# Performance work log

Measured on AMD Instinct MI355X. Metric: run time of the kernel, lower is better.

## Reference

```python
import jax, jax.numpy as jnp
import numpy as np

D_MODEL = 1024
D_INNER = 2048      # expand=2
D_STATE = 128
NHEADS = 32
HEADDIM = 64
DCONV = 4
CONV_DIM = D_INNER + 2 * D_STATE                 # x, B, C channels through conv
D_IN_PROJ = 2 * D_INNER + 2 * D_STATE + NHEADS   # z, xBC, dt
NBLOCKS = 4


def _mlp(x, w1, b1, w2, b2):
    # MLP(2, in, out): Linear(in,in) -> ReLU -> Linear(in,out)
    return jax.nn.relu(x @ w1 + b1) @ w2 + b2


def _mamba2_block(u, Wi, cw, cb, dtb, Alog, Dsk, nw, Wo):
    B, L, _ = u.shape
    zxbcdt = u @ Wi                                        # [B,L,D_IN_PROJ]
    z, xBC, dt = jnp.split(zxbcdt, [D_INNER, D_INNER + CONV_DIM], axis=-1)
    # causal depthwise conv1d, kernel 4
    pad = jnp.pad(xBC, ((0, 0), (DCONV - 1, 0), (0, 0)))
    conv = cb
    for k in range(DCONV):
        conv = conv + pad[:, k:k + L, :] * cw[:, k]
    xBC = jax.nn.silu(conv)
    xh, Bm, Cm = jnp.split(xBC, [D_INNER, D_INNER + D_STATE], axis=-1)
    dt = jax.nn.softplus(dt + dtb)                         # [B,L,H]
    A = -jnp.exp(Alog)                                     # [H], negative
    xh = xh.reshape(B, L, NHEADS, HEADDIM)

    def step(h, inp):
        x_t, dt_t, b_t, c_t = inp                          # [B,H,P],[B,H],[B,N],[B,N]
        dA = jnp.exp(dt_t * A)                             # [B,H]
        h = h * dA[..., None, None] + (dt_t[..., None] * x_t)[..., None] * b_t[:, None, None, :]
        y = jnp.einsum('bhpn,bn->bhp', h, c_t)
        return h, y

    h0 = jnp.zeros((B, NHEADS, HEADDIM, D_STATE), u.dtype)
    _, ys = jax.lax.scan(step, h0, (xh.transpose(1, 0, 2, 3), dt.transpose(1, 0, 2),
                                    Bm.transpose(1, 0, 2), Cm.transpose(1, 0, 2)))
    y = ys.transpose(1, 0, 2, 3) + Dsk[None, None, :, None] * xh   # D skip per head
    y = y.reshape(B, L, D_INNER)
    y = y * jax.nn.silu(z)                                 # gated RMSNorm (gate before norm)
    y = y * jax.lax.rsqrt(jnp.mean(y * y, axis=-1, keepdims=True) + 1e-5) * nw
    return y @ Wo


def setup_inputs() -> dict:
    key = jax.random.key(0)
    ks = jax.random.split(key, 16)
    B, S, STATE = 4, 512, 510
    s = 0.02
    return {
        'x': jax.random.normal(ks[0], (B, S, STATE), jnp.float32),
        'steps_left': jax.random.uniform(ks[1], (B, S, 1), jnp.float32) * 100.0,
        'current_r': jax.random.normal(ks[2], (B, S, 1), jnp.float32),
        'mlp_in_w1': jax.random.normal(ks[3], (STATE + 2, STATE + 2), jnp.float32) * s,
        'mlp_in_b1': jnp.zeros((STATE + 2,), jnp.float32),
        'mlp_in_w2': jax.random.normal(ks[4], (STATE + 2, D_MODEL), jnp.float32) * s,
        'mlp_in_b2': jnp.zeros((D_MODEL,), jnp.float32),
        'W_in': jax.random.normal(ks[5], (NBLOCKS, D_MODEL, D_IN_PROJ), jnp.float32) * s,
        'conv_w': jax.random.normal(ks[6], (NBLOCKS, CONV_DIM, DCONV), jnp.float32) * 0.2,
        'conv_b': jnp.zeros((NBLOCKS, CONV_DIM), jnp.float32),
        'dt_bias': jax.random.normal(ks[7], (NBLOCKS, NHEADS), jnp.float32) * 0.1,
        'A_log': jnp.log(jax.random.uniform(ks[8], (NBLOCKS, NHEADS), jnp.float32, 1.0, 16.0)),
        'D_skip': jnp.ones((NBLOCKS, NHEADS), jnp.float32),
        'norm_w': jnp.ones((NBLOCKS, D_INNER), jnp.float32),
        'W_out': jax.random.normal(ks[9], (NBLOCKS, D_INNER, D_MODEL), jnp.float32) * s,
        'mlp_out_w1': jax.random.normal(ks[10], (D_MODEL, D_MODEL), jnp.float32) * s,
        'mlp_out_b1': jnp.zeros((D_MODEL,), jnp.float32),
        'mlp_out_w2': jax.random.normal(ks[11], (D_MODEL, 1), jnp.float32) * s,
        'mlp_out_b2': jnp.zeros((1,), jnp.float32),
    }


def reference(x, steps_left, current_r,
              mlp_in_w1, mlp_in_b1, mlp_in_w2, mlp_in_b2,
              W_in, conv_w, conv_b, dt_bias, A_log, D_skip, norm_w, W_out,
              mlp_out_w1, mlp_out_b1, mlp_out_w2, mlp_out_b2):
    h = jnp.concatenate([x, steps_left, current_r], axis=-1)   # [B,S,state+2]
    h = _mlp(h, mlp_in_w1, mlp_in_b1, mlp_in_w2, mlp_in_b2)
    for i in range(NBLOCKS):
        h = _mamba2_block(h, W_in[i], conv_w[i], conv_b[i], dt_bias[i],
                          A_log[i], D_skip[i], norm_w[i], W_out[i])
    return _mlp(h, mlp_out_w1, mlp_out_b1, mlp_out_w2, mlp_out_b2)  # [B,S,1]
```

## Files before the change

### kernel.cpp

```cpp
#include <hip/hip_runtime.h>
#include <hip/hip_bf16.h>
#include <math.h>

#define D_MODEL   1024
#define D_INNER   2048
#define D_STATE   128
#define NHEADS    32
#define HEADDIM   64
#define DCONV     4
#define CONV_DIM  (D_INNER + 2 * D_STATE)
#define D_IN_PROJ (2 * D_INNER + 2 * D_STATE + NHEADS)
#define NBLOCKS   4
#define BATCH     4
#define SEQ       512
#define NTOK      (BATCH * SEQ)
#define STATE_IN  510
#define NPAD_IN   4480
#define NSEG      8
#define SEGLEN    64
#define NBH       (BATCH * NHEADS)
#define OFF_B     D_INNER
#define OFF_C     (D_INNER + D_STATE)
#define OFF_DT    (D_IN_PROJ - NHEADS)

typedef _Float16 half8_t __attribute__((ext_vector_type(8)));
typedef float f32x4_t  __attribute__((ext_vector_type(4)));
typedef unsigned short us;
typedef unsigned short us8 __attribute__((ext_vector_type(8)));

__device__ __forceinline__ us f2h(float f) {
    _Float16 h = (_Float16)f;
    return __builtin_bit_cast(us, h);
}
__device__ __forceinline__ float h2f(us u) {
    return (float)__builtin_bit_cast(_Float16, u);
}
__device__ __forceinline__ void gl2lds16(const us* gp, us* lp) {
    __builtin_amdgcn_global_load_lds(
        (const __attribute__((address_space(1))) unsigned int*)(gp),
        (__attribute__((address_space(3))) unsigned int*)(lp), 16, 0, 0);
}

__global__ void concat_kernel(const float* __restrict__ x,
                              const float* __restrict__ steps,
                              const float* __restrict__ curr,
                              us* __restrict__ hcat)
{
    int idx = blockIdx.x * 256 + threadIdx.x;
    if (idx >= NTOK * 512) return;
    int bl = idx >> 9;
    int c  = idx & 511;
    float v;
    if (c < STATE_IN)       v = x[(size_t)bl * STATE_IN + c];
    else if (c == STATE_IN) v = steps[bl];
    else                    v = curr[bl];
    hcat[idx] = f2h(v);
}

#define NT_TRANS 3488
__global__ __launch_bounds__(256)
void transpose_all_kernel(const float* __restrict__ mi_w1, const float* __restrict__ mi_w2,
                          const float* __restrict__ W_in, const float* __restrict__ W_out,
                          const float* __restrict__ mo_w1,
                          us* __restrict__ wt_mi1, us* __restrict__ wt_mi2,
                          us* __restrict__ wt_in, us* __restrict__ wt_out,
                          us* __restrict__ wt_mo1)
{
    int bid = blockIdx.x;
    const float* W; us* WT; int K, N, ntx, r;
    if (bid < 32)        { W = mi_w1; WT = wt_mi1; K = 512;  N = 512;  ntx = 4; r = bid; }
    else if (bid < 96)   { W = mi_w2; WT = wt_mi2; K = 512;  N = 1024; ntx = 8; r = bid - 32; }
    else if (bid < 2336) {
        int rel = bid - 96, i = rel / 560;
        r = rel - i * 560;
        W  = W_in  + (size_t)i * D_MODEL * D_IN_PROJ;
        WT = wt_in + (size_t)i * NPAD_IN * 1024;
        K = 1024; N = D_IN_PROJ; ntx = 35;
    }
    else if (bid < 3360) {
        int rel = bid - 2336, i = rel / 256;
        r = rel - i * 256;
        W  = W_out  + (size_t)i * D_INNER * D_MODEL;
        WT = wt_out + (size_t)i * 1024 * 2048;
        K = 2048; N = 1024; ntx = 8;
    }
    else { W = mo_w1; WT = wt_mo1; K = 1024; N = 1024; ntx = 8; r = bid - 3360; }
    int n0 = (r % ntx) * 128, k0 = (r / ntx) * 64;

    int t = threadIdx.x;
    int ko = t & 7;
    int nq = t >> 3;
    int n  = n0 + nq * 4;
    int k  = k0 + ko * 8;

    float4 v[8];
    if (n < N) {
        const float* src = W + (size_t)k * N + n;
#pragma unroll
        for (int j = 0; j < 8; ++j)
            v[j] = *(const float4*)(src + (size_t)j * N);
    } else {
#pragma unroll
        for (int j = 0; j < 8; ++j) v[j] = make_float4(0.f, 0.f, 0.f, 0.f);
    }
#pragma unroll
    for (int q = 0; q < 4; ++q) {
        us8 o;
#pragma unroll
        for (int j = 0; j < 8; ++j) o[j] = f2h(((const float*)&v[j])[q]);
        *(us8*)(WT + (size_t)(n + q) * K + k) = o;
    }
}

#define PHASE(TT, CUR, STG)                                                     \
    {                                                                           \
        if ((TT) == NT - 1)                                                     \
            asm volatile("s_waitcnt vmcnt(0)" ::: "memory");                    \
        else if constexpr (BM / 64 + BN / 64 == 4)                              \
            asm volatile("s_waitcnt vmcnt(4)" ::: "memory");                    \
        else if constexpr (BM / 64 + BN / 64 == 3)                              \
            asm volatile("s_waitcnt vmcnt(3)" ::: "memory");                    \
        else                                                                    \
            asm volatile("s_waitcnt vmcnt(2)" ::: "memory");                    \
        __builtin_amdgcn_s_barrier();                                           \
        if ((TT) + 2 < NT) stage(STG, ((TT) + 2) << 5);                         \
        half8_t af[TI], bfr[4];                                                 \
        _Pragma("unroll")                                                       \
        for (int ti = 0; ti < TI; ++ti) {                                       \
            int rr = wr + ti * 16 + l16;                                        \
            af[ti] = *(const half8_t*)&Al[CUR][rr * 32 + ((g ^ ((rr >> 2) & 3)) * 8)]; \
        }                                                                       \
        _Pragma("unroll")                                                       \
        for (int tj = 0; tj < 4; ++tj) {                                        \
            int rr = wc + tj * 16 + l16;                                        \
            bfr[tj] = *(const half8_t*)&Bl[CUR][rr * 32 + ((g ^ ((rr >> 2) & 3)) * 8)]; \
        }                                                                       \
        _Pragma("unroll")                                                       \
        for (int ti = 0; ti < TI; ++ti)                                         \
            _Pragma("unroll")                                                   \
            for (int tj = 0; tj < 4; ++tj)                                      \
                acc[ti][tj] = __builtin_amdgcn_mfma_f32_16x16x32_f16(           \
                    af[ti], bfr[tj], acc[ti][tj], 0, 0, 0);                     \
    }

template<int BM, int BN, int TI>
__global__ __launch_bounds__(256)
void mfma_gemm_f16(const us* __restrict__ A, const us* __restrict__ BT,
                   const float* __restrict__ bias, us* __restrict__ C,
                   int N, int K, int relu)
{
    __shared__ __attribute__((aligned(16))) us Al[3][BM * 32];
    __shared__ __attribute__((aligned(16))) us Bl[3][BN * 32];
    const int tid = threadIdx.x, lane = tid & 63, wave = tid >> 6;
    const int g = lane >> 4, l16 = lane & 15;
    const int wr = (BN == 128) ? (wave >> 1) * 64 : wave * (BM / 4);
    const int wc = (BN == 128) ? (wave & 1) * 64 : 0;
    const int m0 = blockIdx.y * BM, n0 = blockIdx.x * BN;
    const int lrow = lane >> 2;
    const int lcol = ((lane & 3) ^ ((lrow >> 2) & 3)) * 8;

    f32x4_t acc[TI][4];
    const f32x4_t zero = {0.f, 0.f, 0.f, 0.f};
#pragma unroll
    for (int i = 0; i < TI; ++i)
#pragma unroll
        for (int j = 0; j < 4; ++j) acc[i][j] = zero;

    const us* abase = A  + (size_t)m0 * K;
    const us* bbase = BT + (size_t)n0 * K;

    auto stage = [&](int buf, int k0) {
#pragma unroll
        for (int s = 0; s < BM / 64; ++s) {
            int rb = wave * (BM / 4) + s * 16;
            gl2lds16(abase + (size_t)(rb + lrow) * K + k0 + lcol, &Al[buf][rb * 32]);
        }
#pragma unroll
        for (int s = 0; s < BN / 64; ++s) {
            int rb = wave * (BN / 4) + s * 16;
            gl2lds16(bbase + (size_t)(rb + lrow) * K + k0 + lcol, &Bl[buf][rb * 32]);
        }
    };

    const int NT = K >> 5;
    stage(0, 0);
    stage(1, 32);

    for (int t = 0; t < NT; t += 3) {
        PHASE(t, 0, 2)
        if (t + 1 < NT) PHASE(t + 1, 1, 0)
        if (t + 2 < NT) PHASE(t + 2, 2, 1)
    }

#pragma unroll
    for (int tj = 0; tj < 4; ++tj) {
        int col = n0 + wc + tj * 16 + l16;
        if (col >= N) continue;
        float bv = bias ? bias[col] : 0.f;
#pragma unroll
        for (int ti = 0; ti < TI; ++ti) {
            int rbase = m0 + wr + ti * 16 + g * 4;
#pragma unroll
            for (int r = 0; r < 4; ++r) {
                float v = acc[ti][tj][r] + bv;
                if (relu) v = fmaxf(v, 0.f);
                C[(size_t)(rbase + r) * N + col] = f2h(v);
            }
        }
    }
}

__global__ __launch_bounds__(256)
void conv_silu_kernel(const us* __restrict__ zxbcdt,
                      const float* __restrict__ cw,
                      const float* __restrict__ cb,
                      us* __restrict__ xBCc)
{
    int idx = blockIdx.x * 256 + threadIdx.x;
    if (idx >= NTOK * (CONV_DIM / 4)) return;
    int cq = idx % (CONV_DIM / 4);
    int bl = idx / (CONV_DIM / 4);
    int b  = bl >> 9;
    int l  = bl & 511;
    int c  = cq * 4;
    float4 w0 = *(const float4*)&cw[(c + 0) * DCONV];
    float4 w1 = *(const float4*)&cw[(c + 1) * DCONV];
    float4 w2 = *(const float4*)&cw[(c + 2) * DCONV];
    float4 w3 = *(const float4*)&cw[(c + 3) * DCONV];
    float4 bb = *(const float4*)&cb[c];
    float a0 = bb.x, a1 = bb.y, a2 = bb.z, a3 = bb.w;
    const us* base = zxbcdt + (size_t)(b * SEQ) * D_IN_PROJ + D_INNER + c;
#pragma unroll
    for (int k = 0; k < DCONV; ++k) {
        int ll = l + k - (DCONV - 1);
        if (ll >= 0) {
            ushort4 u = *(const ushort4*)(base + (size_t)ll * D_IN_PROJ);
            a0 = fmaf(h2f(u.x), ((const float*)&w0)[k], a0);
            a1 = fmaf(h2f(u.y), ((const float*)&w1)[k], a1);
            a2 = fmaf(h2f(u.z), ((const float*)&w2)[k], a2);
            a3 = fmaf(h2f(u.w), ((const float*)&w3)[k], a3);
        }
    }
    ushort4 o;
    o.x = f2h(a0 / (1.f + __expf(-a0)));
    o.y = f2h(a1 / (1.f + __expf(-a1)));
    o.z = f2h(a2 / (1.f + __expf(-a2)));
    o.w = f2h(a3 / (1.f + __expf(-a3)));
    *(ushort4*)(xBCc + (size_t)bl * CONV_DIM + c) = o;
}

__global__ __launch_bounds__(256)
void scan_seg_mfma_kernel(const us* __restrict__ zx, const us* __restrict__ xc,
                          const float* __restrict__ dt_bias,
                          const float* __restrict__ A_log,
                          const float* __restrict__ D_skip,
                          float* __restrict__ y, float* __restrict__ alpha,
                          us* __restrict__ Hseg)
{
    __shared__ __attribute__((aligned(16))) us Csh[64 * 128];
    __shared__ __attribute__((aligned(16))) us Bsh[64 * 128];
    __shared__ __attribute__((aligned(16))) us Bt[128 * 64];
    __shared__ __attribute__((aligned(16))) us Xt[64 * 64];
    __shared__ float dt_s[64], ls[64], csc[64];
    us* Ssh = Csh;
    const int bi = blockIdx.x, bh = bi >> 3, seg = bi & 7;
    const int b = bh >> 5, h = bh & 31;
    const int tid = threadIdx.x, lane = tid & 63, w = tid >> 6;
    const int g = lane >> 4, l16 = lane & 15;
    const int t0g = seg * SEGLEN;
    const size_t rowbase = (size_t)(b * SEQ + t0g);

    {
        int rr = lane >> 4, s = lane & 15;
#pragma unroll
        for (int it = 0; it < 4; ++it) {
            int rb = w * 16 + it * 4;
            int row = rb + rr;
            const us* src = xc + (rowbase + row) * CONV_DIM;
            int sw = (s ^ (row & 7)) * 8;
            gl2lds16(src + OFF_C + sw, &Csh[rb * 128]);
            gl2lds16(src + OFF_B + sw, &Bsh[rb * 128]);
        }
    }
#pragma unroll
    for (int qi = 0; qi < 4; ++qi) {
        int idx = tid + qi * 256;
        int pq = idx & 15, j = idx >> 4;
        ushort4 v = *(const ushort4*)(xc + (rowbase + j) * CONV_DIM + h * 64 + pq * 4);
#pragma unroll
        for (int e = 0; e < 4; ++e) {
            int p = pq * 4 + e;
            int pc = ((((j >> 3) ^ (p & 7)) << 3) | (j & 7));
            Xt[p * 64 + pc] = ((const us*)&v)[e];
        }
    }
#pragma unroll
    for (int qi = 0; qi < 8; ++qi) {
        int idx = tid + qi * 256;
        int nq = idx & 31, j = idx >> 5;
        ushort4 v = *(const ushort4*)(xc + (rowbase + j) * CONV_DIM + OFF_B + nq * 4);
#pragma unroll
        for (int e = 0; e < 4; ++e) {
            int n = nq * 4 + e;
            int pc = ((((j >> 3) ^ (n & 7)) << 3) | (j & 7));
            Bt[n * 64 + pc] = ((const us*)&v)[e];
        }
    }
    if (tid < 64) {
        int j = tid;
        float dtraw = h2f(zx[(rowbase + j) * D_IN_PROJ + OFF_DT + h]) + dt_bias[h];
        float dtv = (dtraw > 20.f) ? dtraw : log1pf(expf(dtraw));
        float ld = dtv * (-expf(A_log[h]));
#pragma unroll
        for (int o = 1; o < 64; o <<= 1) {
            float v = __shfl_up(ld, o);
            if (j >= o) ld += v;
        }
        float al = expf(ld);
        dt_s[j] = dtv;
        ls[j] = ld;
        alpha[(size_t)bh * SEQ + t0g + j] = al;
        float cend = __shfl(ld, 63);
        csc[j] = dtv * expf(cend - ld);
    }
    __syncthreads();

    const float Dsk = D_skip[h];
    const f32x4_t vzero = {0.f, 0.f, 0.f, 0.f};

    f32x4_t acc1[4];
#pragma unroll
    for (int jt = 0; jt < 4; ++jt) acc1[jt] = vzero;
    {
        int ia = w * 16 + l16;
#pragma unroll
        for (int ks = 0; ks < 4; ++ks) {
            half8_t a = *(const half8_t*)&Csh[ia * 128 + (((ks * 4 + g) ^ (ia & 7)) << 3)];
#pragma unroll
            for (int jt = 0; jt < 4; ++jt) {
                int jr = jt * 16 + l16;
                half8_t bfr = *(const half8_t*)&Bsh[jr * 128 + (((ks * 4 + g) ^ (jr & 7)) << 3)];
                acc1[jt] = __builtin_amdgcn_mfma_f32_16x16x32_f16(a, bfr, acc1[jt], 0, 0, 0);
            }
        }
    }
    __syncthreads();

    {
        int i0 = w * 16 + g * 4;
        float lsi[4];
#pragma unroll
        for (int r = 0; r < 4; ++r) lsi[r] = ls[i0 + r];
#pragma unroll
        for (int jt = 0; jt < 4; ++jt) {
            int j = jt * 16 + l16;
            float lj = ls[j], dj = dt_s[j];
#pragma unroll
            for (int r = 0; r < 4; ++r) {
                int i = i0 + r;
                float v = 0.f;
                if (j < i)       v = acc1[jt][r] * dj * __expf(lsi[r] - lj);
                else if (j == i) v = acc1[jt][r] * dj + Dsk;
                int pc = ((((j >> 3) ^ (i & 7)) << 3) | (j & 7));
                Ssh[i * 64 + pc] = f2h(v);
            }
        }
    }
    __syncthreads();

    f32x4_t acc2[4];
#pragma unroll
    for (int nt = 0; nt < 4; ++nt) acc2[nt] = vzero;
    {
        int ia = w * 16 + l16;
#pragma unroll
        for (int ks = 0; ks < 2; ++ks) {
            half8_t a = *(const half8_t*)&Ssh[ia * 64 + (((ks * 4 + g) ^ (ia & 7)) << 3)];
#pragma unroll
            for (int nt = 0; nt < 4; ++nt) {
                int pr = nt * 16 + l16;
                half8_t bfr = *(const half8_t*)&Xt[pr * 64 + (((ks * 4 + g) ^ (pr & 7)) << 3)];
                acc2[nt] = __builtin_amdgcn_mfma_f32_16x16x32_f16(a, bfr, acc2[nt], 0, 0, 0);
            }
        }
    }
    {
        int i0 = w * 16 + g * 4;
#pragma unroll
        for (int nt = 0; nt < 4; ++nt) {
            int p = nt * 16 + l16;
#pragma unroll
            for (int r = 0; r < 4; ++r)
                y[(rowbase + i0 + r) * D_INNER + h * 64 + p] = acc2[nt][r];
        }
    }
    f32x4_t acc3[8];
#pragma unroll
    for (int nt = 0; nt < 8; ++nt) acc3[nt] = vzero;
    {
        int pa = w * 16 + l16;
#pragma unroll
        for (int ks = 0; ks < 2; ++ks) {
            half8_t araw = *(const half8_t*)&Xt[pa * 64 + (((ks * 4 + g) ^ (pa & 7)) << 3)];
            half8_t a;
#pragma unroll
            for (int e = 0; e < 8; ++e)
                a[e] = (_Float16)((float)araw[e] * csc[ks * 32 + g * 8 + e]);
#pragma unroll
            for (int nt = 0; nt < 8; ++nt) {
                int nr = nt * 16 + l16;
                half8_t bfr = *(const half8_t*)&Bt[nr * 64 + (((ks * 4 + g) ^ (nr & 7)) << 3)];
                acc3[nt] = __builtin_amdgcn_mfma_f32_16x16x32_f16(a, bfr, acc3[nt], 0, 0, 0);
            }
        }
    }
    {
        int p0 = w * 16 + g * 4;
#pragma unroll
        for (int nt = 0; nt < 8; ++nt) {
            int n = nt * 16 + l16;
#pragma unroll
            for (int r = 0; r < 4; ++r)
                Hseg[((size_t)bi * 64 + p0 + r) * 128 + n] = f2h(acc3[nt][r]);
        }
    }
}

__global__ __launch_bounds__(512)
void state_fixup_kernel(const float* __restrict__ alpha, us* __restrict__ Hseg)
{
    const int bh = blockIdx.x >> 1, hf = blockIdx.x & 1;
    const int t = threadIdx.x, p = t >> 3, ng = t & 7;
    const int off = hf * 64 + ng * 8;
    float carry[8];
#pragma unroll
    for (int j = 0; j < 8; ++j) carry[j] = 0.f;
    for (int seg = 0; seg < NSEG; ++seg) {
        us* hs = Hseg + (((size_t)bh * NSEG + seg) * 64 + p) * 128 + off;
        float ae = alpha[(size_t)bh * SEQ + seg * SEGLEN + SEGLEN - 1];
        float tmp[8];
#pragma unroll
        for (int q = 0; q < 2; ++q) {
            ushort4 u = *(const ushort4*)(hs + q * 4);
            tmp[q*4+0] = h2f(u.x); tmp[q*4+1] = h2f(u.y);
            tmp[q*4+2] = h2f(u.z); tmp[q*4+3] = h2f(u.w);
        }
#pragma unroll
        for (int q = 0; q < 2; ++q) {
            ushort4 o;
            o.x = f2h(carry[q*4+0]); o.y = f2h(carry[q*4+1]);
            o.z = f2h(carry[q*4+2]); o.w = f2h(carry[q*4+3]);
            *(ushort4*)(hs + q * 4) = o;
        }
#pragma unroll
        for (int j = 0; j < 8; ++j) carry[j] = fmaf(carry[j], ae, tmp[j]);
    }
}

__global__ __launch_bounds__(256)
void correct_mfma_kernel(const us* __restrict__ xc, const float* __restrict__ alpha,
                         const us* __restrict__ Hseg, float* __restrict__ y)
{
    __shared__ __attribute__((aligned(16))) us Csh[64 * 128];
    __shared__ __attribute__((aligned(16))) us Hsh[64 * 128];
    __shared__ float als_s[64];
    const int bi = blockIdx.x;
    const int bh = bi / 7, seg = 1 + (bi % 7);
    const int b = bh >> 5, h = bh & 31;
    const int tid = threadIdx.x, lane = tid & 63, w = tid >> 6;
    const int g = lane >> 4, l16 = lane & 15;
    const int t0g = seg * SEGLEN;
    const size_t rowbase = (size_t)(b * SEQ + t0g);
    const size_t hbase = (size_t)(bh * NSEG + seg) * 64;

    {
        int rr = lane >> 4, s = lane & 15;
#pragma unroll
        for (int it = 0; it < 4; ++it) {
            int rb = w * 16 + it * 4;
            int row = rb + rr;
            int sw = (s ^ (row & 7)) * 8;
            gl2lds16(xc + (rowbase + row) * CONV_DIM + OFF_C + sw, &Csh[rb * 128]);
            gl2lds16(Hseg + (hbase + row) * 128 + sw, &Hsh[rb * 128]);
        }
    }
    if (tid < 64) als_s[tid] = alpha[(size_t)bh * SEQ + t0g + tid];
    __syncthreads();

    const f32x4_t vzero = {0.f, 0.f, 0.f, 0.f};
    f32x4_t acc[4];
#pragma unroll
    for (int nt = 0; nt < 4; ++nt) acc[nt] = vzero;
    int ia = w * 16 + l16;
#pragma unroll
    for (int ks = 0; ks < 4; ++ks) {
        half8_t a = *(const half8_t*)&Csh[ia * 128 + (((ks * 4 + g) ^ (ia & 7)) << 3)];
#pragma unroll
        for (int nt = 0; nt < 4; ++nt) {
            int pr = nt * 16 + l16;
            half8_t bfr = *(const half8_t*)&Hsh[pr * 128 + (((ks * 4 + g) ^ (pr & 7)) << 3)];
            acc[nt] = __builtin_amdgcn_mfma_f32_16x16x32_f16(a, bfr, acc[nt], 0, 0, 0);
        }
    }
    int i0 = w * 16 + g * 4;
#pragma unroll
    for (int nt = 0; nt < 4; ++nt) {
        int p = nt * 16 + l16;
#pragma unroll
        for (int r = 0; r < 4; ++r) {
            size_t idx = (rowbase + i0 + r) * D_INNER + h * 64 + p;
            y[idx] += als_s[i0 + r] * acc[nt][r];
        }
    }
}

__global__ __launch_bounds__(256)
void gated_rmsnorm_kernel(const float* __restrict__ y,
                          const us* __restrict__ zxbcdt,
                          const float* __restrict__ norm_w,
                          us* __restrict__ yn)
{
    int bl = blockIdx.x;
    int t  = threadIdx.x;
    const float* yr = y + (size_t)bl * D_INNER;
    const us* zr = zxbcdt + (size_t)bl * D_IN_PROJ;
    us* outr = yn + (size_t)bl * D_INNER;

    float gv[8];
    float ss = 0.f;
#pragma unroll
    for (int q = 0; q < 8; ++q) {
        int j = t + q * 256;
        float z = h2f(zr[j]);
        float g = yr[j] * (z / (1.f + __expf(-z)));
        gv[q] = g;
        ss += g * g;
    }
    __shared__ float red[256];
    red[t] = ss;
    __syncthreads();
    for (int w = 128; w > 0; w >>= 1) {
        if (t < w) red[t] += red[t + w];
        __syncthreads();
    }
    float rs = rsqrtf(red[0] / (float)D_INNER + 1e-5f);
#pragma unroll
    for (int q = 0; q < 8; ++q) {
        int j = t + q * 256;
        outr[j] = f2h(gv[q] * rs * norm_w[j]);
    }
}

__global__ __launch_bounds__(256)
void final_dot_kernel(const us* __restrict__ t1,
                      const float* __restrict__ w2,
                      const float* __restrict__ b2,
                      float* __restrict__ out)
{
    int bl = blockIdx.x;
    int t  = threadIdx.x;
    float s = 0.f;
    for (int j = t; j < D_MODEL; j += 256)
        s = fmaf(h2f(t1[(size_t)bl * D_MODEL + j]), w2[j], s);
    __shared__ float red[256];
    red[t] = s;
    __syncthreads();
    for (int w = 128; w > 0; w >>= 1) {
        if (t < w) red[t] += red[t + w];
        __syncthreads();
    }
    if (t == 0) out[bl] = red[0] + b2[0];
}

extern "C" void kernel_launch(void* const* d_in, const int* in_sizes, int n_in,
                              void* d_out, int out_size, void* d_ws, size_t ws_size,
                              hipStream_t stream)
{
    const float* x        = (const float*)d_in[0];
    const float* steps    = (const float*)d_in[1];
    const float* curr     = (const float*)d_in[2];
    const float* mi_w1    = (const float*)d_in[3];
    const float* mi_b1    = (const float*)d_in[4];
    const float* mi_w2    = (const float*)d_in[5];
    const float* mi_b2    = (const float*)d_in[6];
    const float* W_in     = (const float*)d_in[7];
    const float* conv_w   = (const float*)d_in[8];
    const float* conv_b   = (const float*)d_in[9];
    const float* dt_bias  = (const float*)d_in[10];
    const float* A_log    = (const float*)d_in[11];
    const float* D_skip   = (const float*)d_in[12];
    const float* norm_w   = (const float*)d_in[13];
    const float* W_out    = (const float*)d_in[14];
    const float* mo_w1    = (const float*)d_in[15];
    const float* mo_b1    = (const float*)d_in[16];
    const float* mo_w2    = (const float*)d_in[17];
    const float* mo_b2    = (const float*)d_in[18];
    float* out = (float*)d_out;

    us* wt_mi1 = (us*)d_ws;
    us* wt_mi2 = wt_mi1 + (size_t)512 * 512;
    us* wt_in  = wt_mi2 + (size_t)1024 * 512;
    us* wt_out = wt_in  + (size_t)4 * NPAD_IN * 1024;
    us* wt_mo1 = wt_out + (size_t)4 * 1024 * 2048;
    us* Hseg   = wt_mo1 + (size_t)1024 * 1024;
    us* hcat   = Hseg   + (size_t)NBH * NSEG * 64 * 128;
    us* h      = hcat   + (size_t)NTOK * 512;
    us* zxb    = h      + (size_t)NTOK * D_MODEL;
    us* xc     = zxb    + (size_t)NTOK * D_IN_PROJ;
    us* yn     = xc     + (size_t)NTOK * CONV_DIM;
    us* t0     = zxb;
    us* t1     = xc;
    float* fbase = (float*)((((uintptr_t)(yn + (size_t)NTOK * D_INNER)) + 255)
                            & ~(uintptr_t)255);
    float* y     = fbase;
    float* alpha = y + (size_t)NTOK * D_INNER;

    transpose_all_kernel<<<NT_TRANS, 256, 0, stream>>>(
        mi_w1, mi_w2, W_in, W_out, mo_w1,
        wt_mi1, wt_mi2, wt_in, wt_out, wt_mo1);

    concat_kernel<<<(NTOK * 512 + 255) / 256, 256, 0, stream>>>(x, steps, curr, hcat);

    mfma_gemm_f16<64, 64, 1><<<dim3(512/64, NTOK/64), 256, 0, stream>>>(
        hcat, wt_mi1, mi_b1, t0, 512, 512, 1);
    mfma_gemm_f16<64, 64, 1><<<dim3(1024/64, NTOK/64), 256, 0, stream>>>(
        t0, wt_mi2, mi_b2, h, 1024, 512, 0);

    for (int i = 0; i < NBLOCKS; ++i) {
        mfma_gemm_f16<128, 128, 4><<<dim3(NPAD_IN/128, NTOK/128), 256, 0, stream>>>(
            h, wt_in + (size_t)i * NPAD_IN * 1024, nullptr, zxb, D_IN_PROJ, D_MODEL, 0);
        conv_silu_kernel<<<(NTOK * (CONV_DIM/4) + 255) / 256, 256, 0, stream>>>(
            zxb, conv_w + (size_t)i * CONV_DIM * DCONV, conv_b + (size_t)i * CONV_DIM, xc);
        scan_seg_mfma_kernel<<<NBH * NSEG, 256, 0, stream>>>(
            zxb, xc, dt_bias + i * NHEADS, A_log + i * NHEADS, D_skip + i * NHEADS,
            y, alpha, Hseg);
        state_fixup_kernel<<<NBH * 2, 512, 0, stream>>>(alpha, Hseg);
        correct_mfma_kernel<<<NBH * (NSEG - 1), 256, 0, stream>>>(xc, alpha, Hseg, y);
        gated_rmsnorm_kernel<<<NTOK, 256, 0, stream>>>(
            y, zxb, norm_w + (size_t)i * D_INNER, yn);
        mfma_gemm_f16<64, 64, 1><<<dim3(1024/64, NTOK/64), 256, 0, stream>>>(
            yn, wt_out + (size_t)i * 1024 * 2048, nullptr, h, 1024, 2048, 0);
    }

    mfma_gemm_f16<64, 64, 1><<<dim3(1024/64, NTOK/64), 256, 0, stream>>>(
        h, wt_mo1, mo_b1, t1, 1024, 1024, 1);
    final_dot_kernel<<<NTOK, 256, 0, stream>>>(t1, mo_w2, mo_b2, out);
}
```

Before: 722.8 us.

## Fuse fp32 weight conversion into GEMM B-tile loads, drop transpose pre-pass

Removes the separate transpose/convert kernel that wrote fp16 transposed copies of every weight matrix. The GEMM now reads fp32 weights directly into registers one tile ahead, converts them to fp16 and writes them swizzled into LDS, while the A tile keeps its async global-to-LDS path. This saves one full read and write of all weights per call, in exchange for more global bytes per B tile, register staging and extra per-tile conversion work inside the GEMM.

```diff
diff --git a/kernel.cpp b/kernel.cpp
--- a/kernel.cpp
+++ b/kernel.cpp
@@ -15,7 +15,6 @@
 #define SEQ       512
 #define NTOK      (BATCH * SEQ)
 #define STATE_IN  510
-#define NPAD_IN   4480
 #define NSEG      8
 #define SEGLEN    64
 #define NBH       (BATCH * NHEADS)
@@ -26,7 +25,6 @@
 typedef _Float16 half8_t __attribute__((ext_vector_type(8)));
 typedef float f32x4_t  __attribute__((ext_vector_type(4)));
 typedef unsigned short us;
-typedef unsigned short us8 __attribute__((ext_vector_type(8)));
 
 __device__ __forceinline__ us f2h(float f) {
     _Float16 h = (_Float16)f;
@@ -57,83 +55,27 @@
     hcat[idx] = f2h(v);
 }
 
-#define NT_TRANS 3488
-__global__ __launch_bounds__(256)
-void transpose_all_kernel(const float* __restrict__ mi_w1, const float* __restrict__ mi_w2,
-                          const float* __restrict__ W_in, const float* __restrict__ W_out,
-                          const float* __restrict__ mo_w1,
-                          us* __restrict__ wt_mi1, us* __restrict__ wt_mi2,
-                          us* __restrict__ wt_in, us* __restrict__ wt_out,
-                          us* __restrict__ wt_mo1)
-{
-    int bid = blockIdx.x;
-    const float* W; us* WT; int K, N, ntx, r;
-    if (bid < 32)        { W = mi_w1; WT = wt_mi1; K = 512;  N = 512;  ntx = 4; r = bid; }
-    else if (bid < 96)   { W = mi_w2; WT = wt_mi2; K = 512;  N = 1024; ntx = 8; r = bid - 32; }
-    else if (bid < 2336) {
-        int rel = bid - 96, i = rel / 560;
-        r = rel - i * 560;
-        W  = W_in  + (size_t)i * D_MODEL * D_IN_PROJ;
-        WT = wt_in + (size_t)i * NPAD_IN * 1024;
-        K = 1024; N = D_IN_PROJ; ntx = 35;
-    }
-    else if (bid < 3360) {
-        int rel = bid - 2336, i = rel / 256;
-        r = rel - i * 256;
-        W  = W_out  + (size_t)i * D_INNER * D_MODEL;
-        WT = wt_out + (size_t)i * 1024 * 2048;
-        K = 2048; N = 1024; ntx = 8;
-    }
-    else { W = mo_w1; WT = wt_mo1; K = 1024; N = 1024; ntx = 8; r = bid - 3360; }
-    int n0 = (r % ntx) * 128, k0 = (r / ntx) * 64;
-
-    int t = threadIdx.x;
-    int ko = t & 7;
-    int nq = t >> 3;
-    int n  = n0 + nq * 4;
-    int k  = k0 + ko * 8;
-
-    float4 v[8];
-    if (n < N) {
-        const float* src = W + (size_t)k * N + n;
-#pragma unroll
-        for (int j = 0; j < 8; ++j)
-            v[j] = *(const float4*)(src + (size_t)j * N);
-    } else {
-#pragma unroll
-        for (int j = 0; j < 8; ++j) v[j] = make_float4(0.f, 0.f, 0.f, 0.f);
-    }
-#pragma unroll
-    for (int q = 0; q < 4; ++q) {
-        us8 o;
-#pragma unroll
-        for (int j = 0; j < 8; ++j) o[j] = f2h(((const float*)&v[j])[q]);
-        *(us8*)(WT + (size_t)(n + q) * K + k) = o;
-    }
-}
-
-#define PHASE(TT, CUR, STG)                                                     \
+#define PHASE(TT, C0, C1, C2, BW, BL)                                           \
     {                                                                           \
-        if ((TT) == NT - 1)                                                     \
-            asm volatile("s_waitcnt vmcnt(0)" ::: "memory");                    \
-        else if constexpr (BM / 64 + BN / 64 == 4)                              \
-            asm volatile("s_waitcnt vmcnt(4)" ::: "memory");                    \
-        else if constexpr (BM / 64 + BN / 64 == 3)                              \
-            asm volatile("s_waitcnt vmcnt(3)" ::: "memory");                    \
-        else                                                                    \
-            asm volatile("s_waitcnt vmcnt(2)" ::: "memory");                    \
+        if ((TT) + 1 < NT) writeB(BW, C1);                                      \
+        asm volatile("s_waitcnt lgkmcnt(0)" ::: "memory");                      \
         __builtin_amdgcn_s_barrier();                                           \
-        if ((TT) + 2 < NT) stage(STG, ((TT) + 2) << 5);                         \
+        __builtin_amdgcn_sched_barrier(0);                                      \
+        if ((TT) + 2 < NT) {                                                    \
+            stageA(C2, ((TT) + 2) << 5);                                        \
+            asm volatile("" ::: "memory");                                      \
+            loadB(BL, ((TT) + 2) << 5);                                         \
+        }                                                                       \
         half8_t af[TI], bfr[4];                                                 \
         _Pragma("unroll")                                                       \
         for (int ti = 0; ti < TI; ++ti) {                                       \
             int rr = wr + ti * 16 + l16;                                        \
-            af[ti] = *(const half8_t*)&Al[CUR][rr * 32 + ((g ^ ((rr >> 2) & 3)) * 8)]; \
+            af[ti] = *(const half8_t*)&Al[C0][rr * 32 + ((g ^ ((rr >> 2) & 3)) * 8)]; \
         }                                                                       \
         _Pragma("unroll")                                                       \
         for (int tj = 0; tj < 4; ++tj) {                                        \
             int rr = wc + tj * 16 + l16;                                        \
-            bfr[tj] = *(const half8_t*)&Bl[CUR][rr * 32 + ((g ^ ((rr >> 2) & 3)) * 8)]; \
+            bfr[tj] = *(const half8_t*)&Bl[C0][rr * 32 + ((g ^ ((rr >> 2) & 3)) * 8)]; \
         }                                                                       \
         _Pragma("unroll")                                                       \
         for (int ti = 0; ti < TI; ++ti)                                         \
@@ -145,7 +87,7 @@
 
 template<int BM, int BN, int TI>
 __global__ __launch_bounds__(256)
-void mfma_gemm_f16(const us* __restrict__ A, const us* __restrict__ BT,
+void mfma_gemm_f16(const us* __restrict__ A, const float* __restrict__ W,
                    const float* __restrict__ bias, us* __restrict__ C,
                    int N, int K, int relu)
 {
@@ -159,6 +101,14 @@
     const int lrow = lane >> 2;
     const int lcol = ((lane & 3) ^ ((lrow >> 2) & 3)) * 8;
 
+    constexpr int NQ = (BN == 128) ? 32 : 16;
+    constexpr int KR = (BN == 128) ? 4  : 2;
+    const int nq = tid & (NQ - 1);
+    const int kk = tid / NQ;
+    const int nn = n0 + nq * 4;
+    const int gB = (kk * KR) >> 3;
+    const int e0 = (kk * KR) & 7;
+
     f32x4_t acc[TI][4];
     const f32x4_t zero = {0.f, 0.f, 0.f, 0.f};
 #pragma unroll
@@ -166,30 +116,65 @@
 #pragma unroll
         for (int j = 0; j < 4; ++j) acc[i][j] = zero;
 
-    const us* abase = A  + (size_t)m0 * K;
-    const us* bbase = BT + (size_t)n0 * K;
-
-    auto stage = [&](int buf, int k0) {
+    const us* abase = A + (size_t)m0 * K;
+    float4 br0[KR], br1[KR];
+
+    auto stageA = [&](int buf, int k0) {
 #pragma unroll
         for (int s = 0; s < BM / 64; ++s) {
             int rb = wave * (BM / 4) + s * 16;
             gl2lds16(abase + (size_t)(rb + lrow) * K + k0 + lcol, &Al[buf][rb * 32]);
         }
-#pragma unroll
-        for (int s = 0; s < BN / 64; ++s) {
-            int rb = wave * (BN / 4) + s * 16;
-            gl2lds16(bbase + (size_t)(rb + lrow) * K + k0 + lcol, &Bl[buf][rb * 32]);
-        }
     };
+    auto loadB = [&](float4* br, int k0) {
+        if (nn < N) {
+            const float* src = W + (size_t)(k0 + kk * KR) * N + nn;
+#pragma unroll
+            for (int dk = 0; dk < KR; ++dk)
+                br[dk] = *(const float4*)(src + (size_t)dk * N);
+        } else {
+#pragma unroll
+            for (int dk = 0; dk < KR; ++dk)
+                br[dk] = make_float4(0.f, 0.f, 0.f, 0.f);
+        }
+    };
+    auto writeB = [&](float4* br, int buf) {
+        us* bl = &Bl[buf][0];
+#pragma unroll
+        for (int q = 0; q < 4; ++q) {
+            us* dst = bl + (nq * 4 + q) * 32 + (gB ^ (nq & 3)) * 8 + e0;
+            if constexpr (KR == 4) {
+                ushort4 o;
+                o.x = f2h(((const float*)&br[0])[q]);
+                o.y = f2h(((const float*)&br[1])[q]);
+                o.z = f2h(((const float*)&br[2])[q]);
+                o.w = f2h(((const float*)&br[3])[q]);
+                *(ushort4*)dst = o;
+            } else {
+                unsigned int v = (unsigned int)f2h(((const float*)&br[0])[q])
+                               | ((unsigned int)f2h(((const float*)&br[1])[q]) << 16);
+                *(unsigned int*)dst = v;
+            }
+        }
+    };
 
     const int NT = K >> 5;
-    stage(0, 0);
-    stage(1, 32);
-
-    for (int t = 0; t < NT; t += 3) {
-        PHASE(t, 0, 2)
-        if (t + 1 < NT) PHASE(t + 1, 1, 0)
-        if (t + 2 < NT) PHASE(t + 2, 2, 1)
+    stageA(0, 0);
+    asm volatile("" ::: "memory");
+    loadB(br0, 0);
+    asm volatile("" ::: "memory");
+    stageA(1, 32);
+    asm volatile("" ::: "memory");
+    loadB(br1, 32);
+    writeB(br0, 0);
+
+    for (int t = 0; t < NT; t += 6) {
+        PHASE(t,     0, 1, 2, br1, br0)
+        if (t + 1 < NT) PHASE(t + 1, 1, 2, 0, br0, br1)
+        if (t + 2 < NT) PHASE(t + 2, 2, 0, 1, br1, br0)
+        if (t + 3 < NT) PHASE(t + 3, 0, 1, 2, br0, br1)
+        if (t + 4 < NT) PHASE(t + 4, 1, 2, 0, br1, br0)
+        if (t + 5 < NT) PHASE(t + 5, 2, 0, 1, br0, br1)
     }
 
 #pragma unroll
@@ -597,38 +582,29 @@
     const float* mo_b2    = (const float*)d_in[18];
     float* out = (float*)d_out;
 
-    us* wt_mi1 = (us*)d_ws;
-    us* wt_mi2 = wt_mi1 + (size_t)512 * 512;
-    us* wt_in  = wt_mi2 + (size_t)1024 * 512;
-    us* wt_out = wt_in  + (size_t)4 * NPAD_IN * 1024;
-    us* wt_mo1 = wt_out + (size_t)4 * 1024 * 2048;
-    us* Hseg   = wt_mo1 + (size_t)1024 * 1024;
-    us* hcat   = Hseg   + (size_t)NBH * NSEG * 64 * 128;
-    us* h      = hcat   + (size_t)NTOK * 512;
-    us* zxb    = h      + (size_t)NTOK * D_MODEL;
-    us* xc     = zxb    + (size_t)NTOK * D_IN_PROJ;
-    us* yn     = xc     + (size_t)NTOK * CONV_DIM;
-    us* t0     = zxb;
-    us* t1     = xc;
+    us* Hseg = (us*)d_ws;
+    us* hcat = Hseg + (size_t)NBH * NSEG * 64 * 128;
+    us* h    = hcat + (size_t)NTOK * 512;
+    us* zxb  = h    + (size_t)NTOK * D_MODEL;
+    us* xc   = zxb  + (size_t)NTOK * D_IN_PROJ;
+    us* yn   = xc   + (size_t)NTOK * CONV_DIM;
+    us* t0   = zxb;
+    us* t1   = xc;
     float* fbase = (float*)((((uintptr_t)(yn + (size_t)NTOK * D_INNER)) + 255)
                             & ~(uintptr_t)255);
     float* y     = fbase;
     float* alpha = y + (size_t)NTOK * D_INNER;
 
-    transpose_all_kernel<<<NT_TRANS, 256, 0, stream>>>(
-        mi_w1, mi_w2, W_in, W_out, mo_w1,
-        wt_mi1, wt_mi2, wt_in, wt_out, wt_mo1);
-
     concat_kernel<<<(NTOK * 512 + 255) / 256, 256, 0, stream>>>(x, steps, curr, hcat);
 
     mfma_gemm_f16<64, 64, 1><<<dim3(512/64, NTOK/64), 256, 0, stream>>>(
-        hcat, wt_mi1, mi_b1, t0, 512, 512, 1);
+        hcat, mi_w1, mi_b1, t0, 512, 512, 1);
     mfma_gemm_f16<64, 64, 1><<<dim3(1024/64, NTOK/64), 256, 0, stream>>>(
-        t0, wt_mi2, mi_b2, h, 1024, 512, 0);
+        t0, mi_w2, mi_b2, h, 1024, 512, 0);
 
     for (int i = 0; i < NBLOCKS; ++i) {
-        mfma_gemm_f16<128, 128, 4><<<dim3(NPAD_IN/128, NTOK/128), 256, 0, stream>>>(
-            h, wt_in + (size_t)i * NPAD_IN * 1024, nullptr, zxb, D_IN_PROJ, D_MODEL, 0);
+        mfma_gemm_f16<128, 128, 4><<<dim3((D_IN_PROJ + 127) / 128, NTOK/128), 256, 0, stream>>>(
+            h, W_in + (size_t)i * D_MODEL * D_IN_PROJ, nullptr, zxb, D_IN_PROJ, D_MODEL, 0);
         conv_silu_kernel<<<(NTOK * (CONV_DIM/4) + 255) / 256, 256, 0, stream>>>(
             zxb, conv_w + (size_t)i * CONV_DIM * DCONV, conv_b + (size_t)i * CONV_DIM, xc);
         scan_seg_mfma_kernel<<<NBH * NSEG, 256, 0, stream>>>(
@@ -639,10 +615,10 @@
         gated_rmsnorm_kernel<<<NTOK, 256, 0, stream>>>(
             y, zxb, norm_w + (size_t)i * D_INNER, yn);
         mfma_gemm_f16<64, 64, 1><<<dim3(1024/64, NTOK/64), 256, 0, stream>>>(
-            yn, wt_out + (size_t)i * 1024 * 2048, nullptr, h, 1024, 2048, 0);
+            yn, W_out + (size_t)i * D_INNER * D_MODEL, nullptr, h, 1024, 2048, 0);
     }
 
     mfma_gemm_f16<64, 64, 1><<<dim3(1024/64, NTOK/64), 256, 0, stream>>>(
-        h, wt_mo1, mo_b1, t1, 1024, 1024, 1);
+        h, mo_w1, mo_b1, t1, 1024, 1024, 1);
     final_dot_kernel<<<NTOK, 256, 0, stream>>>(t1, mo_w2, mo_b2, out);
 }
```

Result: slower. 833.3 us (+15.3%).
